# Kernel optimization log

Hardware: AMD Instinct MI355X
Metric: run time of the kernel (lower is better)

The kernel has to match this reference:

```python
import jax, jax.numpy as jnp
import numpy as np

B, N, E, H, MAXLEN = 64, 256, 1024, 16, 512
D = E // H
LN_EPS = 1e-5
NORM_EPS = 1e-12


def setup_inputs() -> dict:
    key = jax.random.key(0)
    ks = jax.random.split(key, 12)
    s = 1.0 / np.sqrt(E)
    return {
        "news_embeds": jax.random.normal(ks[0], (B, N, E), jnp.float32),
        "padding_mask": jax.random.uniform(ks[1], (B, N)) > 0.8,  # True = padded
        "cls_token": jax.random.normal(ks[2], (1, 1, E), jnp.float32),
        "pos_emb": jax.random.normal(ks[3], (MAXLEN + 1, E), jnp.float32) * 0.02,
        "in_proj_w": jax.random.normal(ks[4], (3 * E, E), jnp.float32) * s,
        "in_proj_b": jnp.zeros((3 * E,), jnp.float32),
        "out_proj_w": jax.random.normal(ks[5], (E, E), jnp.float32) * s,
        "out_proj_b": jnp.zeros((E,), jnp.float32),
        "proj_w": jax.random.normal(ks[6], (E, E), jnp.float32) * s,
        "proj_b": jnp.zeros((E,), jnp.float32),
        "ln_gamma": jnp.ones((E,), jnp.float32),
        "ln_beta": jnp.zeros((E,), jnp.float32),
    }


def reference(news_embeds, padding_mask, cls_token, pos_emb, in_proj_w, in_proj_b,
              out_proj_w, out_proj_b, proj_w, proj_b, ln_gamma, ln_beta):
    b, n, e = news_embeds.shape
    S = n + 1
    # prepend CLS token, add positional encodings (dropout inactive in eval)
    x = jnp.concatenate([jnp.broadcast_to(cls_token, (b, 1, e)), news_embeds], axis=1)
    x = x + pos_emb[:S][None, :, :]
    # key padding mask with CLS always attendable
    mask = jnp.concatenate(
        [jnp.zeros((b, 1), dtype=bool), padding_mask], axis=1)  # [b,S]
    # packed QKV projection (nn.MultiheadAttention in_proj)
    qkv = jnp.einsum('bse,fe->bsf', x, in_proj_w) + in_proj_b
    q, k, v = jnp.split(qkv, 3, axis=-1)
    q = q.reshape(b, S, H, D)
    k = k.reshape(b, S, H, D)
    v = v.reshape(b, S, H, D)
    scores = jnp.einsum('bqhd,bkhd->bhqk', q, k) / jnp.sqrt(
        jnp.asarray(D, x.dtype))
    big_neg = jnp.asarray(-1e9, scores.dtype)
    scores = jnp.where(mask[:, None, None, :], big_neg, scores)
    attn = jax.nn.softmax(scores, axis=-1)  # [b,H,S,S]
    ctx = jnp.einsum('bhqk,bkhd->bqhd', attn, v).reshape(b, S, e)
    attn_out = jnp.einsum('bse,fe->bsf', ctx, out_proj_w) + out_proj_b
    # projection head: Linear -> (Dropout eval noop) -> LayerNorm -> ReLU
    p = jnp.einsum('bse,fe->bsf', attn_out, proj_w) + proj_b
    mu = jnp.mean(p, axis=-1, keepdims=True)
    var = jnp.var(p, axis=-1, keepdims=True)
    ln = (p - mu) * jax.lax.rsqrt(var + LN_EPS) * ln_gamma + ln_beta
    proj = jax.nn.relu(ln)
    user = proj[:, 0, :]
    norm = jnp.maximum(jnp.linalg.norm(user, axis=-1, keepdims=True), NORM_EPS)
    user = user / norm
    return user, attn
```

## Files before the change

### kernel.cpp

```cpp
#include <hip/hip_runtime.h>

#define B_   64
#define N_   256
#define E_   1024
#define H_   16
#define D_   64
#define S_   257
#define M_   16448
#define MP2  16640
#define N3_  3072
#define K_   1024

typedef unsigned short u16;
typedef unsigned int   u32;
typedef __bf16 bf16x8 __attribute__((ext_vector_type(8)));
typedef float  f32x4  __attribute__((ext_vector_type(4)));

__device__ inline u16 f2bf(float f) {
  union { float f; u32 u; } a; a.f = f;
  return (u16)((a.u + 0x7FFFu + ((a.u >> 16) & 1u)) >> 16);
}
__device__ inline float bf2f(u16 h) {
  union { u32 u; float f; } a; a.u = ((u32)h) << 16; return a.f;
}
__device__ inline void gload_lds16(const void* g, void* l) {
  __builtin_amdgcn_global_load_lds((const __attribute__((address_space(1))) void*)g,
                                   (__attribute__((address_space(3))) void*)l, 16, 0, 0);
}

__global__ __launch_bounds__(256) void prep_w(const float* __restrict__ w, u16* __restrict__ o) {
  size_t i = ((size_t)blockIdx.x * 256 + threadIdx.x) * 4;
  float4 f = *(const float4*)(w + i);
  ushort4 v;
  v.x = f2bf(f.x); v.y = f2bf(f.y); v.z = f2bf(f.z); v.w = f2bf(f.w);
  *(ushort4*)(o + i) = v;
}

__global__ __launch_bounds__(256) void build_x(const float* __restrict__ news,
                                               const float* __restrict__ cls,
                                               const float* __restrict__ pos,
                                               u16* __restrict__ x) {
  const int row = blockIdx.x;
  const int e = threadIdx.x * 4;
  float4 v = make_float4(0.f, 0.f, 0.f, 0.f);
  if (row < M_) {
    const int b = row / S_;
    const int s = row - b * S_;
    float4 pe = *(const float4*)(pos + (size_t)s * E_ + e);
    float4 xv = (s == 0) ? *(const float4*)(cls + e)
                         : *(const float4*)(news + ((size_t)b * N_ + (s - 1)) * E_ + e);
    v.x = xv.x + pe.x; v.y = xv.y + pe.y; v.z = xv.z + pe.z; v.w = xv.w + pe.w;
  }
  ushort4 o;
  o.x = f2bf(v.x); o.y = f2bf(v.y); o.z = f2bf(v.z); o.w = f2bf(v.w);
  *(ushort4*)(x + (size_t)row * E_ + e) = o;
}

__global__ __launch_bounds__(256) void mask_prep(const void* __restrict__ src, int* __restrict__ dst) {
  const int t = threadIdx.x;
  const u32* wsrc = (const u32*)src;
  u32 flag = 0;
  for (int i = t; i < 4096; i += 256) {
    u32 v = wsrc[i];
    if (v == 0x3F800000u) flag |= 2u;
    else if (v > 1u) flag |= 1u;
  }
  __shared__ u32 fsh;
  if (t == 0) fsh = 0;
  __syncthreads();
  if (flag) atomicOr(&fsh, flag);
  __syncthreads();
  const u32 f = fsh;
  const int mode = (f & 2u) ? 2 : ((f & 1u) ? 1 : 0);
  const int base = blockIdx.x * 2048;
  for (int i = base + t; i < base + 2048; i += 256) {
    int m;
    if (mode == 0)      m = (wsrc[i] != 0u);
    else if (mode == 2) m = (((const float*)src)[i] != 0.f);
    else                m = (((const unsigned char*)src)[i] != 0);
    dst[i] = m;
  }
}

__global__ __launch_bounds__(256) void gemm_qkv(const u16* __restrict__ A,
                                                const u16* __restrict__ Bw,
                                                const float* __restrict__ bias,
                                                u16* __restrict__ C) {
  __shared__ u16 As[128 * 32];
  __shared__ u16 Bs[128 * 32];
  const int t = threadIdx.x;
  const int w = t >> 6, l = t & 63;
  const int wr = w >> 1, wc = w & 1;

  const int orig = blockIdx.x;
  const int wgid = (orig & 7) * 390 + (orig >> 3);
  const int bm = wgid / 24, bn = wgid % 24;

  const u16* Ab = A + (size_t)bm * 128 * K_;
  const u16* Bb = Bw + (size_t)bn * 128 * K_;
  f32x4 acc[4][4] = {};
  const int r0 = t >> 2,         col0 = (t & 3) << 3;
  const int r1 = (256 + t) >> 2, col1 = ((256 + t) & 3) << 3;
  char* AsB = (char*)As + w * 1024;
  char* BsB = (char*)Bs + w * 1024;

  for (int k0 = 0; k0 < K_; k0 += 32) {
    gload_lds16(Ab + (size_t)r0 * K_ + k0 + col0, AsB);
    gload_lds16(Ab + (size_t)r1 * K_ + k0 + col1, AsB + 4096);
    gload_lds16(Bb + (size_t)r0 * K_ + k0 + col0, BsB);
    gload_lds16(Bb + (size_t)r1 * K_ + k0 + col1, BsB + 4096);
    __syncthreads();
    const int kc = (l >> 4) << 3;
    bf16x8 af[4], bfr[4];
#pragma unroll
    for (int m = 0; m < 4; ++m)
      af[m] = *(const bf16x8*)&As[(wr * 64 + m * 16 + (l & 15)) * 32 + kc];
#pragma unroll
    for (int n = 0; n < 4; ++n)
      bfr[n] = *(const bf16x8*)&Bs[(wc * 64 + n * 16 + (l & 15)) * 32 + kc];
#pragma unroll
    for (int m = 0; m < 4; ++m)
#pragma unroll
      for (int n = 0; n < 4; ++n)
        acc[m][n] = __builtin_amdgcn_mfma_f32_16x16x32_bf16(af[m], bfr[n], acc[m][n], 0, 0, 0);
    __syncthreads();
  }
  const int row0 = bm * 128 + wr * 64 + ((l >> 4) << 2);
  const int colb = bn * 128 + wc * 64 + (l & 15);
#pragma unroll
  for (int n = 0; n < 4; ++n) {
    const int col = colb + n * 16;
    const float bv = bias[col];
#pragma unroll
    for (int m = 0; m < 4; ++m) {
      const int row = row0 + m * 16;
#pragma unroll
      for (int j = 0; j < 4; ++j)
        C[(size_t)(row + j) * N3_ + col] = f2bf(acc[m][n][j] + bv);
    }
  }
}

__global__ __launch_bounds__(256) void attn_kernel(const u16* __restrict__ qkv,
                                                   const int* __restrict__ maskw,
                                                   float* __restrict__ attn,
                                                   float* __restrict__ ctx) {
  __shared__ u16 Ks[272 * 72];
  __shared__ u16 Qs[64 * 72];
  __shared__ float msk[272];
  __shared__ float p0[272];
  __shared__ float red[4][64];
  const int qt = blockIdx.x, h = blockIdx.y, b = blockIdx.z;
  const int t = threadIdx.x;
  const int q0 = qt * 64;

  for (int c = t; c < 272 * 8; c += 256) {
    const int r = c >> 3, qq = c & 7;
    uint4 val = make_uint4(0, 0, 0, 0);
    if (r < S_)
      val = *(const uint4*)(qkv + (size_t)(b * S_ + r) * N3_ + E_ + h * 64 + qq * 8);
    *(uint4*)&Ks[r * 72 + qq * 8] = val;
  }
  for (int c = t; c < 64 * 8; c += 256) {
    const int r = c >> 3, qq = c & 7;
    const int gq = q0 + r;
    uint4 val = make_uint4(0, 0, 0, 0);
    if (gq < S_)
      val = *(const uint4*)(qkv + (size_t)(b * S_ + gq) * N3_ + h * 64 + qq * 8);
    *(uint4*)&Qs[r * 72 + qq * 8] = val;
  }
  for (int i = t; i < 272; i += 256) {
    float m = 0.f;
    if (i == 0) m = 1.f;
    else if (i < S_) m = maskw[b * N_ + i - 1] ? 0.f : 1.f;
    msk[i] = m;
  }
  __syncthreads();

  const int w = t >> 6, l = t & 63;
  const int cl = l & 15, rg = l >> 4;
  const int kc = rg * 8;

  const u16* qbase = &Qs[(w * 16 + cl) * 72 + kc];
  const bf16x8 qb0 = *(const bf16x8*)qbase;
  const bf16x8 qb1 = *(const bf16x8*)(qbase + 32);

  float ev[17][4];
  float sum = 0.f;
#pragma unroll
  for (int kt = 0; kt < 17; ++kt) {
    const u16* kbase = &Ks[(kt * 16 + cl) * 72 + kc];
    f32x4 a = {0.f, 0.f, 0.f, 0.f};
    a = __builtin_amdgcn_mfma_f32_16x16x32_bf16(*(const bf16x8*)kbase, qb0, a, 0, 0, 0);
    a = __builtin_amdgcn_mfma_f32_16x16x32_bf16(*(const bf16x8*)(kbase + 32), qb1, a, 0, 0, 0);
    const f32x4 m4 = *(const f32x4*)&msk[kt * 16 + rg * 4];
#pragma unroll
    for (int j = 0; j < 4; ++j) {
      const float e = m4[j] * __expf(a[j] * 0.125f);
      ev[kt][j] = e;
      sum += e;
    }
  }
  sum += __shfl_xor(sum, 16);
  sum += __shfl_xor(sum, 32);
  const float inv = 1.f / sum;

  const int gq = q0 + w * 16 + cl;
  if (gq < S_) {
    float* arow = attn + (size_t)((b * H_ + h) * S_ + gq) * S_;
#pragma unroll
    for (int kt = 0; kt < 16; ++kt) {
      f32x4 v;
      v[0] = ev[kt][0] * inv; v[1] = ev[kt][1] * inv;
      v[2] = ev[kt][2] * inv; v[3] = ev[kt][3] * inv;
      __builtin_memcpy(arow + kt * 16 + rg * 4, &v, 16);
    }
    if (rg == 0) arow[256] = ev[16][0] * inv;
  }

  if (qt == 0) {
    if (w == 0 && cl == 0) {
#pragma unroll
      for (int kt = 0; kt < 17; ++kt)
#pragma unroll
        for (int j = 0; j < 4; ++j)
          p0[kt * 16 + rg * 4 + j] = ev[kt][j] * inv;
    }
    __syncthreads();
    const int part = t >> 6, d = t & 63;
    float acc = 0.f;
    for (int k = part; k < S_; k += 4)
      acc = fmaf(p0[k], bf2f(qkv[(size_t)(b * S_ + k) * N3_ + 2 * E_ + h * 64 + d]), acc);
    red[part][d] = acc;
    __syncthreads();
    if (t < 64)
      ctx[(size_t)b * E_ + h * 64 + t] = red[0][t] + red[1][t] + red[2][t] + red[3][t];
  }
}

__global__ __launch_bounds__(256) void gemv_cls(const float* __restrict__ in,
                                                const float* __restrict__ W,
                                                const float* __restrict__ bias,
                                                float* __restrict__ out) {
  const int bt = blockIdx.x, fc = blockIdx.y, t = threadIdx.x;
  __shared__ float xs[4][E_];
  for (int i = t; i < E_; i += 256)
    ((float4*)xs)[i] = ((const float4*)(in + (size_t)bt * 4 * E_))[i];
  __syncthreads();
  const int f = fc * 64 + (t >> 2);
  const int ec = (t & 3) * 256;
  const float4* wr = (const float4*)(W + (size_t)f * E_ + ec);
  float a0 = 0.f, a1 = 0.f, a2 = 0.f, a3 = 0.f;
#pragma unroll 8
  for (int e4 = 0; e4 < 64; ++e4) {
    const float4 wv = wr[e4];
    const float4 x0 = *(const float4*)&xs[0][ec + e4 * 4];
    const float4 x1 = *(const float4*)&xs[1][ec + e4 * 4];
    const float4 x2 = *(const float4*)&xs[2][ec + e4 * 4];
    const float4 x3 = *(const float4*)&xs[3][ec + e4 * 4];
    a0 += wv.x * x0.x + wv.y * x0.y + wv.z * x0.z + wv.w * x0.w;
    a1 += wv.x * x1.x + wv.y * x1.y + wv.z * x1.z + wv.w * x1.w;
    a2 += wv.x * x2.x + wv.y * x2.y + wv.z * x2.z + wv.w * x2.w;
    a3 += wv.x * x3.x + wv.y * x3.y + wv.z * x3.z + wv.w * x3.w;
  }
  a0 += __shfl_xor(a0, 1); a0 += __shfl_xor(a0, 2);
  a1 += __shfl_xor(a1, 1); a1 += __shfl_xor(a1, 2);
  a2 += __shfl_xor(a2, 1); a2 += __shfl_xor(a2, 2);
  a3 += __shfl_xor(a3, 1); a3 += __shfl_xor(a3, 2);
  if ((t & 3) == 0) {
    const float bv = bias[f];
    out[(size_t)(bt * 4 + 0) * E_ + f] = a0 + bv;
    out[(size_t)(bt * 4 + 1) * E_ + f] = a1 + bv;
    out[(size_t)(bt * 4 + 2) * E_ + f] = a2 + bv;
    out[(size_t)(bt * 4 + 3) * E_ + f] = a3 + bv;
  }
}

__global__ __launch_bounds__(256) void ln_relu_norm(const float* __restrict__ p,
                                                    const float* __restrict__ gamma,
                                                    const float* __restrict__ beta,
                                                    float* __restrict__ user) {
  const int b = blockIdx.x, t = threadIdx.x;
  const int w = t >> 6, l = t & 63;
  const float4 v = ((const float4*)(p + (size_t)b * E_))[t];
  float s = v.x + v.y + v.z + v.w;
  float s2 = v.x * v.x + v.y * v.y + v.z * v.z + v.w * v.w;
#pragma unroll
  for (int o = 1; o < 64; o <<= 1) { s += __shfl_xor(s, o); s2 += __shfl_xor(s2, o); }
  __shared__ float ss[4], ss2[4], qs[4];
  if (l == 0) { ss[w] = s; ss2[w] = s2; }
  __syncthreads();
  s = ss[0] + ss[1] + ss[2] + ss[3];
  s2 = ss2[0] + ss2[1] + ss2[2] + ss2[3];
  const float mu = s * (1.f / E_);
  const float var = s2 * (1.f / E_) - mu * mu;
  const float rstd = rsqrtf(var + 1e-5f);
  const float4 g = ((const float4*)gamma)[t];
  const float4 be = ((const float4*)beta)[t];
  float4 o;
  o.x = fmaxf((v.x - mu) * rstd * g.x + be.x, 0.f);
  o.y = fmaxf((v.y - mu) * rstd * g.y + be.y, 0.f);
  o.z = fmaxf((v.z - mu) * rstd * g.z + be.z, 0.f);
  o.w = fmaxf((v.w - mu) * rstd * g.w + be.w, 0.f);
  float q2 = o.x * o.x + o.y * o.y + o.z * o.z + o.w * o.w;
#pragma unroll
  for (int off = 1; off < 64; off <<= 1) q2 += __shfl_xor(q2, off);
  if (l == 0) qs[w] = q2;
  __syncthreads();
  q2 = qs[0] + qs[1] + qs[2] + qs[3];
  const float nrm = fmaxf(sqrtf(q2), 1e-12f);
  const float inv = 1.f / nrm;
  float4 u;
  u.x = o.x * inv; u.y = o.y * inv; u.z = o.z * inv; u.w = o.w * inv;
  ((float4*)(user + (size_t)b * E_))[t] = u;
}

extern "C" void kernel_launch(void* const* d_in, const int* in_sizes, int n_in,
                              void* d_out, int out_size, void* d_ws, size_t ws_size,
                              hipStream_t stream) {
  const float* news   = (const float*)d_in[0];
  const void*  maskp  = d_in[1];
  const float* cls    = (const float*)d_in[2];
  const float* pos    = (const float*)d_in[3];
  const float* w_in   = (const float*)d_in[4];
  const float* b_in   = (const float*)d_in[5];
  const float* w_out  = (const float*)d_in[6];
  const float* b_out  = (const float*)d_in[7];
  const float* w_proj = (const float*)d_in[8];
  const float* b_proj = (const float*)d_in[9];
  const float* gamma  = (const float*)d_in[10];
  const float* beta   = (const float*)d_in[11];

  char* ws = (char*)d_ws;
  u16*  w_bf  = (u16*)(ws + 0);
  u16*  x_bf  = (u16*)(ws + 6291456);
  u16*  qkv   = (u16*)(ws + 40370176);
  float* ctx  = (float*)(ws + 142606336);
  float* aoc  = (float*)(ws + 142868480);
  float* pcls = (float*)(ws + 143130624);
  int*  maskw = (int*)(ws + 143392768);

  float* user = (float*)d_out;
  float* attn = (float*)d_out + (size_t)B_ * E_;

  prep_w<<<3072, 256, 0, stream>>>(w_in, w_bf);
  build_x<<<MP2, 256, 0, stream>>>(news, cls, pos, x_bf);
  mask_prep<<<8, 256, 0, stream>>>(maskp, maskw);
  gemm_qkv<<<3120, 256, 0, stream>>>(x_bf, w_bf, b_in, qkv);
  attn_kernel<<<dim3(5, H_, B_), 256, 0, stream>>>(qkv, maskw, attn, ctx);
  gemv_cls<<<dim3(16, 16), 256, 0, stream>>>(ctx, w_out, b_out, aoc);
  gemv_cls<<<dim3(16, 16), 256, 0, stream>>>(aoc, w_proj, b_proj, pcls);
  ln_relu_norm<<<B_, 256, 0, stream>>>(pcls, gamma, beta, user);
}
```

Measured before the change: 367.0 us.

## Merge query tiles into one 1024-thread attention block per head and batch

New measurement: 464.2 us. +26.5%, slower.

```diff
diff --git a/kernel.cpp b/kernel.cpp
--- a/kernel.cpp
+++ b/kernel.cpp
@@ -141,35 +141,25 @@
   }
 }
 
-__global__ __launch_bounds__(256) void attn_kernel(const u16* __restrict__ qkv,
-                                                   const int* __restrict__ maskw,
-                                                   float* __restrict__ attn,
-                                                   float* __restrict__ ctx) {
+__global__ __launch_bounds__(1024, 8) void attn_kernel(const u16* __restrict__ qkv,
+                                                       const int* __restrict__ maskw,
+                                                       float* __restrict__ attn,
+                                                       float* __restrict__ ctx) {
   __shared__ u16 Ks[272 * 72];
-  __shared__ u16 Qs[64 * 72];
   __shared__ float msk[272];
   __shared__ float p0[272];
-  __shared__ float red[4][64];
-  const int qt = blockIdx.x, h = blockIdx.y, b = blockIdx.z;
+  __shared__ float red[16][64];
+  const int h = blockIdx.x, b = blockIdx.y;
   const int t = threadIdx.x;
-  const int q0 = qt * 64;
-
-  for (int c = t; c < 272 * 8; c += 256) {
+
+  for (int c = t; c < 272 * 8; c += 1024) {
     const int r = c >> 3, qq = c & 7;
     uint4 val = make_uint4(0, 0, 0, 0);
     if (r < S_)
       val = *(const uint4*)(qkv + (size_t)(b * S_ + r) * N3_ + E_ + h * 64 + qq * 8);
     *(uint4*)&Ks[r * 72 + qq * 8] = val;
   }
-  for (int c = t; c < 64 * 8; c += 256) {
-    const int r = c >> 3, qq = c & 7;
-    const int gq = q0 + r;
-    uint4 val = make_uint4(0, 0, 0, 0);
-    if (gq < S_)
-      val = *(const uint4*)(qkv + (size_t)(b * S_ + gq) * N3_ + h * 64 + qq * 8);
-    *(uint4*)&Qs[r * 72 + qq * 8] = val;
-  }
-  for (int i = t; i < 272; i += 256) {
+  for (int i = t; i < 272; i += 1024) {
     float m = 0.f;
     if (i == 0) m = 1.f;
     else if (i < S_) m = maskw[b * N_ + i - 1] ? 0.f : 1.f;
@@ -181,60 +171,70 @@
   const int cl = l & 15, rg = l >> 4;
   const int kc = rg * 8;
 
-  const u16* qbase = &Qs[(w * 16 + cl) * 72 + kc];
-  const bf16x8 qb0 = *(const bf16x8*)qbase;
-  const bf16x8 qb1 = *(const bf16x8*)(qbase + 32);
-
-  float ev[17][4];
-  float sum = 0.f;
-#pragma unroll
-  for (int kt = 0; kt < 17; ++kt) {
-    const u16* kbase = &Ks[(kt * 16 + cl) * 72 + kc];
-    f32x4 a = {0.f, 0.f, 0.f, 0.f};
-    a = __builtin_amdgcn_mfma_f32_16x16x32_bf16(*(const bf16x8*)kbase, qb0, a, 0, 0, 0);
-    a = __builtin_amdgcn_mfma_f32_16x16x32_bf16(*(const bf16x8*)(kbase + 32), qb1, a, 0, 0, 0);
-    const f32x4 m4 = *(const f32x4*)&msk[kt * 16 + rg * 4];
-#pragma unroll
-    for (int j = 0; j < 4; ++j) {
-      const float e = m4[j] * __expf(a[j] * 0.125f);
-      ev[kt][j] = e;
-      sum += e;
+  for (int g = w; g < 17; g += 16) {
+    const int gq = g * 16 + cl;
+    const u16* qrow = qkv + (size_t)(b * S_ + gq) * N3_ + h * 64 + kc;
+    const bf16x8 qb0 = *(const bf16x8*)qrow;
+    const bf16x8 qb1 = *(const bf16x8*)(qrow + 32);
+
+    const bool ok = (gq < S_);
+    float* arow = attn + (size_t)((b * H_ + h) * S_ + gq) * S_;
+
+    float sum = 0.f, eLast = 0.f;
+#pragma unroll
+    for (int kt = 0; kt < 17; ++kt) {
+      const u16* kbase = &Ks[(kt * 16 + cl) * 72 + kc];
+      f32x4 a = {0.f, 0.f, 0.f, 0.f};
+      a = __builtin_amdgcn_mfma_f32_16x16x32_bf16(*(const bf16x8*)kbase, qb0, a, 0, 0, 0);
+      a = __builtin_amdgcn_mfma_f32_16x16x32_bf16(*(const bf16x8*)(kbase + 32), qb1, a, 0, 0, 0);
+      const f32x4 m4 = *(const f32x4*)&msk[kt * 16 + rg * 4];
+      f32x4 e;
+#pragma unroll
+      for (int j = 0; j < 4; ++j) {
+        e[j] = m4[j] * __expf(a[j] * 0.125f);
+        sum += e[j];
+      }
+      if (kt < 16) {
+        if (ok) __builtin_memcpy(arow + kt * 16 + rg * 4, &e, 16);
+      } else {
+        eLast = e[0];
+      }
     }
-  }
-  sum += __shfl_xor(sum, 16);
-  sum += __shfl_xor(sum, 32);
-  const float inv = 1.f / sum;
-
-  const int gq = q0 + w * 16 + cl;
-  if (gq < S_) {
-    float* arow = attn + (size_t)((b * H_ + h) * S_ + gq) * S_;
-#pragma unroll
-    for (int kt = 0; kt < 16; ++kt) {
-      f32x4 v;
-      v[0] = ev[kt][0] * inv; v[1] = ev[kt][1] * inv;
-      v[2] = ev[kt][2] * inv; v[3] = ev[kt][3] * inv;
-      __builtin_memcpy(arow + kt * 16 + rg * 4, &v, 16);
+    sum += __shfl_xor(sum, 16);
+    sum += __shfl_xor(sum, 32);
+    const float inv = 1.f / sum;
+
+    asm volatile("s_waitcnt vmcnt(0)" ::: "memory");
+    const bool isCls = (g == 0 && cl == 0);
+    if (ok) {
+#pragma unroll
+      for (int kt = 0; kt < 16; ++kt) {
+        f32x4 v;
+        __builtin_memcpy(&v, arow + kt * 16 + rg * 4, 16);
+        v[0] *= inv; v[1] *= inv; v[2] *= inv; v[3] *= inv;
+        __builtin_memcpy(arow + kt * 16 + rg * 4, &v, 16);
+        if (isCls) {
+#pragma unroll
+          for (int j = 0; j < 4; ++j) p0[kt * 16 + rg * 4 + j] = v[j];
+        }
+      }
+      if (rg == 0) arow[256] = eLast * inv;
     }
-    if (rg == 0) arow[256] = ev[16][0] * inv;
-  }
-
-  if (qt == 0) {
-    if (w == 0 && cl == 0) {
-#pragma unroll
-      for (int kt = 0; kt < 17; ++kt)
-#pragma unroll
-        for (int j = 0; j < 4; ++j)
-          p0[kt * 16 + rg * 4 + j] = ev[kt][j] * inv;
-    }
-    __syncthreads();
-    const int part = t >> 6, d = t & 63;
-    float acc = 0.f;
-    for (int k = part; k < S_; k += 4)
-      acc = fmaf(p0[k], bf2f(qkv[(size_t)(b * S_ + k) * N3_ + 2 * E_ + h * 64 + d]), acc);
-    red[part][d] = acc;
-    __syncthreads();
-    if (t < 64)
-      ctx[(size_t)b * E_ + h * 64 + t] = red[0][t] + red[1][t] + red[2][t] + red[3][t];
+    if (isCls && rg == 0) p0[256] = eLast * inv;
+  }
+
+  __syncthreads();
+  const int part = t >> 6, d = t & 63;
+  float acc = 0.f;
+  for (int k = part; k < S_; k += 16)
+    acc = fmaf(p0[k], bf2f(qkv[(size_t)(b * S_ + k) * N3_ + 2 * E_ + h * 64 + d]), acc);
+  red[part][d] = acc;
+  __syncthreads();
+  if (t < 64) {
+    float s = 0.f;
+#pragma unroll
+    for (int i = 0; i < 16; ++i) s += red[i][t];
+    ctx[(size_t)b * E_ + h * 64 + t] = s;
   }
 }
 
@@ -347,7 +347,7 @@
   build_x<<<MP2, 256, 0, stream>>>(news, cls, pos, x_bf);
   mask_prep<<<8, 256, 0, stream>>>(maskp, maskw);
   gemm_qkv<<<3120, 256, 0, stream>>>(x_bf, w_bf, b_in, qkv);
-  attn_kernel<<<dim3(5, H_, B_), 256, 0, stream>>>(qkv, maskw, attn, ctx);
+  attn_kernel<<<dim3(H_, B_), 1024, 0, stream>>>(qkv, maskw, attn, ctx);
   gemv_cls<<<dim3(16, 16), 256, 0, stream>>>(ctx, w_out, b_out, aoc);
   gemv_cls<<<dim3(16, 16), 256, 0, stream>>>(aoc, w_proj, b_proj, pcls);
   ln_relu_norm<<<B_, 256, 0, stream>>>(pcls, gamma, beta, user);
```
